# Kernel tuning notes

Measured on AMD Instinct MI355X. Metric: run time of the kernel, lower is better.

The kernel has to match this reference:

```python
import jax, jax.numpy as jnp
import numpy as np
import math

B, H_IM, W_IM, HDIM, HEADS, PS = 16, 56, 56, 512, 8, 7


def setup_inputs() -> dict:
    key = jax.random.key(0)
    ks = jax.random.split(key, 4)
    x = jax.random.normal(ks[0], (B, H_IM * W_IM, HDIM), jnp.float32)
    mask = jnp.zeros((1, 1, H_IM, W_IM), jnp.bool_)
    Wqkv = jax.random.normal(ks[1], (HDIM, 3 * HDIM), jnp.float32) * 0.02
    Wproj = jax.random.normal(ks[2], (HDIM, HDIM), jnp.float32) * 0.02
    bproj = jnp.zeros((HDIM,), jnp.float32)
    rel_bias = jax.random.normal(ks[3], (HEADS, PS * PS, PS * PS), jnp.float32) * 0.02
    return {"x": x, "mask": mask, "Wqkv": Wqkv, "Wproj": Wproj,
            "bproj": bproj, "rel_bias": rel_bias, "H": H_IM, "W": W_IM}


def reference(x, mask, Wqkv, Wproj, bproj, rel_bias, H, W):
    b = x.shape[0]
    ps, g, hd = PS, HEADS, HDIM
    dh = hd // g
    scale = dh ** (-0.5)

    qkv = x @ Wqkv                                   # [b, H*W, 3*hd]
    qkv = qkv.reshape(b, H, W, 3 * hd)
    pad_b = int(math.ceil(H / ps)) * ps - H
    pad_r = int(math.ceil(W / ps)) * ps - W
    qkv = jnp.pad(qkv, ((0, 0), (0, pad_b), (0, pad_r), (0, 0)))
    kmask = jnp.pad(mask, ((0, 0), (0, 0), (0, pad_b), (0, pad_r)), constant_values=True)
    Hp, Wp = H + pad_b, W + pad_r
    sh, sw = Hp // ps, Wp // ps
    K, P = ps * ps, sh * sw

    # patchify: b (sh kh) (sw kw) c -> b (kh kw) (sh sw) c
    qkv = qkv.reshape(b, sh, ps, sw, ps, 3 * hd).transpose(0, 2, 4, 1, 3, 5).reshape(b, K, P, 3 * hd)
    kmask = kmask.reshape(1, 1, sh, ps, sw, ps).transpose(0, 1, 3, 5, 2, 4).reshape(1, 1, K, P)

    qkv = qkv.reshape(b, K, P, 3, g, dh)
    q, k, v = qkv[:, :, :, 0], qkv[:, :, :, 1], qkv[:, :, :, 2]  # each [b, K, P, g, dh]

    attn = jnp.einsum('bqpgc,bkpgc->bgqkp', q, k)    # [b, g, K, K, P]
    attn = (attn + rel_bias[None, :, :, :, None]) * scale
    m = kmask[:, None]                                # [1, 1, 1, K, P]
    attn = jnp.where(m, -jnp.inf, attn)
    attn = jax.nn.softmax(attn, axis=-2)              # softmax over key positions within window
    attn = jnp.where(m, 0.0, attn)

    out = jnp.einsum('bgqkp,bkpgc->bqpgc', attn, v)
    out = out.reshape(b, K, P, hd)
    # un-patchify: b (kh kw) (sh sw) c -> b (sh kh) (sw kw) c
    out = out.reshape(b, ps, ps, sh, sw, hd).transpose(0, 3, 1, 4, 2, 5).reshape(b, Hp, Wp, hd)
    out = out[:, :H, :W, :].reshape(b, H * W, hd)
    return out @ Wproj + bproj
```

## Files before the change

### kernel.cpp

```cpp
#include <hip/hip_runtime.h>
#include <hip/hip_bf16.h>

using bf16 = __hip_bfloat16;
using bf16x8 = __attribute__((ext_vector_type(8))) short;
using f32x4  = __attribute__((ext_vector_type(4))) float;

#define B_    16
#define HIM   56
#define WIM   56
#define HD    512
#define NHEAD 8
#define DH    64
#define NTOK  (HIM*WIM)
#define M_    (B_*NTOK)
#define K49   49

__device__ __forceinline__ void gload_lds16(const void* g, void* l) {
  __builtin_amdgcn_global_load_lds(
      (__attribute__((address_space(1))) const void*)g,
      (__attribute__((address_space(3))) void*)l, 16, 0, 0);
}

__global__ __launch_bounds__(256) void cvt_x_kernel(const float* __restrict__ in,
                                                    bf16* __restrict__ out) {
  size_t i = ((size_t)blockIdx.x * 256 + threadIdx.x) * 8;
  float4 a = *(const float4*)(in + i);
  float4 b = *(const float4*)(in + i + 4);
  union { uint4 v; bf16 h[8]; } o;
  o.h[0] = __float2bfloat16(a.x); o.h[1] = __float2bfloat16(a.y);
  o.h[2] = __float2bfloat16(a.z); o.h[3] = __float2bfloat16(a.w);
  o.h[4] = __float2bfloat16(b.x); o.h[5] = __float2bfloat16(b.y);
  o.h[6] = __float2bfloat16(b.z); o.h[7] = __float2bfloat16(b.w);
  *(uint4*)(out + i) = o.v;
}

__global__ __launch_bounds__(256) void cvt_transpose_kernel(const float* __restrict__ in,
                                                            bf16* __restrict__ out,
                                                            int K, int N) {
  int idx = blockIdx.x * 256 + threadIdx.x;
  int k = idx / N, n = idx - k * N;
  out[(size_t)n * K + k] = __float2bfloat16(in[idx]);
}

template<bool OUT_BF16, bool BIAS>
__global__ __launch_bounds__(256) void gemm128_kernel(
    const bf16* __restrict__ A,
    const bf16* __restrict__ Bt,
    void* __restrict__ Cp,
    const float* __restrict__ bias,
    int M, int N, int K)
{
  __shared__ alignas(16) bf16 lds[2][2][128 * 32];
  const int tid  = threadIdx.x;
  const int lane = tid & 63, wid = tid >> 6;
  const int l15  = lane & 15, kq = lane >> 4;
  const int wm   = wid >> 1,  wn = wid & 1;
  const long arow0 = (long)blockIdx.y * 128;
  const long bcol0 = (long)blockIdx.x * 128;

  auto stage = [&](int buf, int kt) {
    const bf16* gA = A  + arow0 * K + kt * 32;
    const bf16* gB = Bt + bcol0 * K + kt * 32;
#pragma unroll
    for (int c = 0; c < 2; ++c) {
      int s   = c * 256 + tid;
      int row = s >> 2, sl = s & 3;
      int gs  = sl ^ ((row >> 1) & 3);
      const char* pa = (const char*)(gA + (long)row * K) + gs * 16;
      const char* pb = (const char*)(gB + (long)row * K) + gs * 16;
      bf16* la = (bf16*)&lds[buf][0][(c * 256 + wid * 64) * 8];
      bf16* lb = (bf16*)&lds[buf][1][(c * 256 + wid * 64) * 8];
      gload_lds16(pa, la);
      gload_lds16(pb, lb);
    }
  };

  f32x4 acc[4][4] = {};
  stage(0, 0);
  __syncthreads();
  const int nk = K >> 5;
  int buf = 0;
#pragma unroll 1
  for (int kt = 0; kt < nk; ++kt) {
    if (kt + 1 < nk) stage(buf ^ 1, kt + 1);
    bf16x8 af[4], br[4];
#pragma unroll
    for (int mt = 0; mt < 4; ++mt) {
      int row  = wm * 64 + mt * 16 + l15;
      int slot = kq ^ ((row >> 1) & 3);
      af[mt] = *(const bf16x8*)&lds[buf][0][row * 32 + slot * 8];
    }
#pragma unroll
    for (int nt = 0; nt < 4; ++nt) {
      int row  = wn * 64 + nt * 16 + l15;
      int slot = kq ^ ((row >> 1) & 3);
      br[nt] = *(const bf16x8*)&lds[buf][1][row * 32 + slot * 8];
    }
#pragma unroll
    for (int mt = 0; mt < 4; ++mt)
#pragma unroll
      for (int nt = 0; nt < 4; ++nt)
        acc[mt][nt] = __builtin_amdgcn_mfma_f32_16x16x32_bf16(af[mt], br[nt], acc[mt][nt], 0, 0, 0);
    __syncthreads();
    buf ^= 1;
  }

  const long crow0 = arow0 + wm * 64;
  const long ccol0 = bcol0 + wn * 64;
#pragma unroll
  for (int mt = 0; mt < 4; ++mt) {
#pragma unroll
    for (int nt = 0; nt < 4; ++nt) {
      long col = ccol0 + nt * 16 + l15;
      float bv = BIAS ? bias[col] : 0.f;
#pragma unroll
      for (int r = 0; r < 4; ++r) {
        long row = crow0 + mt * 16 + kq * 4 + r;
        if (OUT_BF16)
          ((bf16*)Cp)[row * N + col] = __float2bfloat16(acc[mt][nt][r]);
        else
          ((float*)Cp)[row * N + col] = acc[mt][nt][r] + bv;
      }
    }
  }
}

__global__ __launch_bounds__(256) void attn_win_kernel(
    const bf16* __restrict__ qkv, const float* __restrict__ rb, bf16* __restrict__ outa)
{
  __shared__ alignas(16) bf16 Qs[64 * 72];
  __shared__ alignas(16) bf16 Ks[64 * 72];
  __shared__ alignas(16) bf16 Vt[64 * 72];
  __shared__ alignas(16) bf16 Ps[64 * 72];
  const int tid = threadIdx.x, lane = tid & 63, wid = tid >> 6;
  const int p = blockIdx.x, g = blockIdx.y, b = blockIdx.z;
  const int sh = p >> 3, sw = p & 7;
  const size_t nb = (size_t)b * NTOK;
  const int c8 = (tid & 7) * 8;

#pragma unroll
  for (int it = 0; it < 2; ++it) {
    int t = (tid >> 3) + it * 32;
    uint4 vq = {0, 0, 0, 0}, vk = vq, vv = vq;
    if (t < K49) {
      int ph = t / 7, pw = t - ph * 7;
      int n = (sh * 7 + ph) * WIM + sw * 7 + pw;
      const bf16* src = qkv + (nb + n) * 1536 + g * 64 + c8;
      vq = *(const uint4*)(src);
      vk = *(const uint4*)(src + 512);
      vv = *(const uint4*)(src + 1024);
    }
    *(uint4*)&Qs[t * 72 + c8] = vq;
    *(uint4*)&Ks[t * 72 + c8] = vk;
    union { uint4 u; unsigned short s[8]; } uv; uv.u = vv;
    unsigned short* vt16 = (unsigned short*)Vt;
#pragma unroll
    for (int e = 0; e < 8; ++e) vt16[(c8 + e) * 72 + t] = uv.s[e];
  }
  __syncthreads();

  const int l15 = lane & 15, kq = lane >> 4;
  bf16x8 aq[2];
#pragma unroll
  for (int kk = 0; kk < 2; ++kk)
    aq[kk] = *(const bf16x8*)&Qs[(wid * 16 + l15) * 72 + kk * 32 + kq * 8];
  float sv[4][4];
#pragma unroll
  for (int ct = 0; ct < 4; ++ct) {
    f32x4 acc = {0.f, 0.f, 0.f, 0.f};
#pragma unroll
    for (int kk = 0; kk < 2; ++kk) {
      bf16x8 bk = *(const bf16x8*)&Ks[(ct * 16 + l15) * 72 + kk * 32 + kq * 8];
      acc = __builtin_amdgcn_mfma_f32_16x16x32_bf16(aq[kk], bk, acc, 0, 0, 0);
    }
    int kcol = ct * 16 + l15;
#pragma unroll
    for (int r = 0; r < 4; ++r) {
      int q = wid * 16 + kq * 4 + r;
      float bias = (q < K49 && kcol < K49) ? rb[((size_t)g * K49 + q) * K49 + kcol] : 0.f;
      float v = (acc[r] + bias) * 0.125f;
      sv[ct][r] = (kcol < K49) ? v : -1e30f;
    }
  }
#pragma unroll
  for (int r = 0; r < 4; ++r) {
    float m = fmaxf(fmaxf(sv[0][r], sv[1][r]), fmaxf(sv[2][r], sv[3][r]));
#pragma unroll
    for (int d = 1; d < 16; d <<= 1) m = fmaxf(m, __shfl_xor(m, d));
    float e0 = __expf(sv[0][r] - m), e1 = __expf(sv[1][r] - m);
    float e2 = __expf(sv[2][r] - m), e3 = __expf(sv[3][r] - m);
    float s = e0 + e1 + e2 + e3;
#pragma unroll
    for (int d = 1; d < 16; d <<= 1) s += __shfl_xor(s, d);
    float inv = 1.0f / s;
    int q = wid * 16 + kq * 4 + r;
    Ps[q * 72 +  0 + l15] = __float2bfloat16(e0 * inv);
    Ps[q * 72 + 16 + l15] = __float2bfloat16(e1 * inv);
    Ps[q * 72 + 32 + l15] = __float2bfloat16(e2 * inv);
    Ps[q * 72 + 48 + l15] = __float2bfloat16(e3 * inv);
  }
  __syncthreads();
  bf16x8 ap[2];
#pragma unroll
  for (int kk = 0; kk < 2; ++kk)
    ap[kk] = *(const bf16x8*)&Ps[(wid * 16 + l15) * 72 + kk * 32 + kq * 8];
#pragma unroll
  for (int ct = 0; ct < 4; ++ct) {
    f32x4 acc = {0.f, 0.f, 0.f, 0.f};
#pragma unroll
    for (int kk = 0; kk < 2; ++kk) {
      bf16x8 bv = *(const bf16x8*)&Vt[(ct * 16 + l15) * 72 + kk * 32 + kq * 8];
      acc = __builtin_amdgcn_mfma_f32_16x16x32_bf16(ap[kk], bv, acc, 0, 0, 0);
    }
#pragma unroll
    for (int r = 0; r < 4; ++r) {
      int q = wid * 16 + kq * 4 + r;
      if (q < K49) {
        int ph = q / 7, pw = q - ph * 7;
        int n = (sh * 7 + ph) * WIM + sw * 7 + pw;
        outa[(nb + n) * HD + g * 64 + ct * 16 + l15] = __float2bfloat16(acc[r]);
      }
    }
  }
}

extern "C" void kernel_launch(void* const* d_in, const int* in_sizes, int n_in,
                              void* d_out, int out_size, void* d_ws, size_t ws_size,
                              hipStream_t stream) {
  (void)in_sizes; (void)n_in; (void)out_size;
  const float* x     = (const float*)d_in[0];
  const float* wqkv  = (const float*)d_in[2];
  const float* wproj = (const float*)d_in[3];
  const float* bproj = (const float*)d_in[4];
  const float* rb    = (const float*)d_in[5];

  char* ws = (char*)d_ws;
  bf16* x_bf    = (bf16*)(ws);
  bf16* wqkv_t  = (bf16*)(ws + 51380224);
  bf16* wproj_t = (bf16*)(ws + 52953088);
  bf16* qkv     = (bf16*)(ws + 53477376);
  bf16* attno   = x_bf;
  float* out    = (float*)d_out;
  if (ws_size < 207618048) return;

  cvt_x_kernel<<<dim3(12544), 256, 0, stream>>>(x, x_bf);
  cvt_transpose_kernel<<<dim3(3072), 256, 0, stream>>>(wqkv, wqkv_t, 512, 1536);
  cvt_transpose_kernel<<<dim3(1024), 256, 0, stream>>>(wproj, wproj_t, 512, 512);
  gemm128_kernel<true, false><<<dim3(12, 392), 256, 0, stream>>>(
      x_bf, wqkv_t, (void*)qkv, nullptr, M_, 1536, 512);
  attn_win_kernel<<<dim3(64, NHEAD, B_), 256, 0, stream>>>(qkv, rb, attno);
  gemm128_kernel<false, true><<<dim3(4, 392), 256, 0, stream>>>(
      attno, wproj_t, (void*)out, bproj, M_, 512, 512);
}
```

Baseline: 254.5 us.

## Triple-buffer GEMM pipeline with XCD-aware block remap and nontemporal stores

The GEMM kernel moves from double to triple LDS buffering, prefetching two k-tiles ahead and waiting with explicit vmcnt counts before a single barrier per iteration, in place of two syncthreads. The 2D grid becomes a 1D grid remapped so that consecutive tiles land on the same XCD, to improve L2 reuse. It also raises wave priority around the MFMA block and writes outputs with nontemporal stores. The costs are extra LDS per block (48KB, still within 3 blocks/CU) and reliance on hand-written waitcnt counts being correct.

```diff
diff --git a/kernel.cpp b/kernel.cpp
--- a/kernel.cpp
+++ b/kernel.cpp
@@ -43,20 +43,23 @@
 }
 
 template<bool OUT_BF16, bool BIAS>
-__global__ __launch_bounds__(256) void gemm128_kernel(
+__global__ __launch_bounds__(256, 3) void gemm128_kernel(
     const bf16* __restrict__ A,
     const bf16* __restrict__ Bt,
     void* __restrict__ Cp,
     const float* __restrict__ bias,
-    int M, int N, int K)
+    int M, int N, int K, int NBX)
 {
-  __shared__ alignas(16) bf16 lds[2][2][128 * 32];
+  __shared__ alignas(16) bf16 lds[3][2][128 * 32];
   const int tid  = threadIdx.x;
   const int lane = tid & 63, wid = tid >> 6;
   const int l15  = lane & 15, kq = lane >> 4;
   const int wm   = wid >> 1,  wn = wid & 1;
-  const long arow0 = (long)blockIdx.y * 128;
-  const long bcol0 = (long)blockIdx.x * 128;
+  const int cpx = gridDim.x >> 3;
+  const int wg  = (blockIdx.x & 7) * cpx + (blockIdx.x >> 3);
+  const int by  = wg / NBX, bx = wg - by * NBX;
+  const long arow0 = (long)by * 128;
+  const long bcol0 = (long)bx * 128;
 
   auto stage = [&](int buf, int kt) {
     const bf16* gA = A  + arow0 * K + kt * 32;
@@ -66,43 +69,47 @@
       int s   = c * 256 + tid;
       int row = s >> 2, sl = s & 3;
       int gs  = sl ^ ((row >> 1) & 3);
-      const char* pa = (const char*)(gA + (long)row * K) + gs * 16;
-      const char* pb = (const char*)(gB + (long)row * K) + gs * 16;
-      bf16* la = (bf16*)&lds[buf][0][(c * 256 + wid * 64) * 8];
-      bf16* lb = (bf16*)&lds[buf][1][(c * 256 + wid * 64) * 8];
-      gload_lds16(pa, la);
-      gload_lds16(pb, lb);
+      gload_lds16((const char*)(gA + (long)row * K) + gs * 16,
+                  (bf16*)&lds[buf][0][(c * 256 + wid * 64) * 8]);
+      gload_lds16((const char*)(gB + (long)row * K) + gs * 16,
+                  (bf16*)&lds[buf][1][(c * 256 + wid * 64) * 8]);
     }
   };
 
   f32x4 acc[4][4] = {};
+  const int NT = K >> 5;
   stage(0, 0);
-  __syncthreads();
-  const int nk = K >> 5;
-  int buf = 0;
+  stage(1, 1);
+  int cur = 0;
 #pragma unroll 1
-  for (int kt = 0; kt < nk; ++kt) {
-    if (kt + 1 < nk) stage(buf ^ 1, kt + 1);
+  for (int t = 0; t < NT; ++t) {
+    if (t + 1 < NT) asm volatile("s_waitcnt vmcnt(4)" ::: "memory");
+    else            asm volatile("s_waitcnt vmcnt(0)" ::: "memory");
+    __builtin_amdgcn_s_barrier();
+    asm volatile("" ::: "memory");
+    if (t + 2 < NT) { int nb = cur + 2; if (nb >= 3) nb -= 3; stage(nb, t + 2); }
+
     bf16x8 af[4], br[4];
 #pragma unroll
     for (int mt = 0; mt < 4; ++mt) {
       int row  = wm * 64 + mt * 16 + l15;
       int slot = kq ^ ((row >> 1) & 3);
-      af[mt] = *(const bf16x8*)&lds[buf][0][row * 32 + slot * 8];
-    }
-#pragma unroll
-    for (int nt = 0; nt < 4; ++nt) {
-      int row  = wn * 64 + nt * 16 + l15;
+      af[mt] = *(const bf16x8*)&lds[cur][0][row * 32 + slot * 8];
+    }
+#pragma unroll
+    for (int nt2 = 0; nt2 < 4; ++nt2) {
+      int row  = wn * 64 + nt2 * 16 + l15;
       int slot = kq ^ ((row >> 1) & 3);
-      br[nt] = *(const bf16x8*)&lds[buf][1][row * 32 + slot * 8];
-    }
+      br[nt2] = *(const bf16x8*)&lds[cur][1][row * 32 + slot * 8];
+    }
+    __builtin_amdgcn_s_setprio(1);
 #pragma unroll
     for (int mt = 0; mt < 4; ++mt)
 #pragma unroll
-      for (int nt = 0; nt < 4; ++nt)
-        acc[mt][nt] = __builtin_amdgcn_mfma_f32_16x16x32_bf16(af[mt], br[nt], acc[mt][nt], 0, 0, 0);
-    __syncthreads();
-    buf ^= 1;
+      for (int nt2 = 0; nt2 < 4; ++nt2)
+        acc[mt][nt2] = __builtin_amdgcn_mfma_f32_16x16x32_bf16(af[mt], br[nt2], acc[mt][nt2], 0, 0, 0);
+    __builtin_amdgcn_s_setprio(0);
+    ++cur; if (cur >= 3) cur = 0;
   }
 
   const long crow0 = arow0 + wm * 64;
@@ -110,16 +117,19 @@
 #pragma unroll
   for (int mt = 0; mt < 4; ++mt) {
 #pragma unroll
-    for (int nt = 0; nt < 4; ++nt) {
-      long col = ccol0 + nt * 16 + l15;
+    for (int nt2 = 0; nt2 < 4; ++nt2) {
+      long col = ccol0 + nt2 * 16 + l15;
       float bv = BIAS ? bias[col] : 0.f;
 #pragma unroll
       for (int r = 0; r < 4; ++r) {
         long row = crow0 + mt * 16 + kq * 4 + r;
-        if (OUT_BF16)
-          ((bf16*)Cp)[row * N + col] = __float2bfloat16(acc[mt][nt][r]);
-        else
-          ((float*)Cp)[row * N + col] = acc[mt][nt][r] + bv;
+        if (OUT_BF16) {
+          bf16 h = __float2bfloat16(acc[mt][nt2][r]);
+          __builtin_nontemporal_store(*(const unsigned short*)&h,
+                                      (unsigned short*)Cp + row * N + col);
+        } else {
+          __builtin_nontemporal_store(acc[mt][nt2][r] + bv, (float*)Cp + row * N + col);
+        }
       }
     }
   }
@@ -246,9 +256,9 @@
   cvt_x_kernel<<<dim3(12544), 256, 0, stream>>>(x, x_bf);
   cvt_transpose_kernel<<<dim3(3072), 256, 0, stream>>>(wqkv, wqkv_t, 512, 1536);
   cvt_transpose_kernel<<<dim3(1024), 256, 0, stream>>>(wproj, wproj_t, 512, 512);
-  gemm128_kernel<true, false><<<dim3(12, 392), 256, 0, stream>>>(
-      x_bf, wqkv_t, (void*)qkv, nullptr, M_, 1536, 512);
+  gemm128_kernel<true, false><<<dim3(4704), 256, 0, stream>>>(
+      x_bf, wqkv_t, (void*)qkv, nullptr, M_, 1536, 512, 12);
   attn_win_kernel<<<dim3(64, NHEAD, B_), 256, 0, stream>>>(qkv, rb, attno);
-  gemm128_kernel<false, true><<<dim3(4, 392), 256, 0, stream>>>(
-      attno, wproj_t, (void*)out, bproj, M_, 512, 512);
-}
+  gemm128_kernel<false, true><<<dim3(1568), 256, 0, stream>>>(
+      attno, wproj_t, (void*)out, bproj, M_, 512, 512, 4);
+}
```

Measured after the change: 250.9 us. No clear change (-1.4%).

## Replace 128x128 GEMM with persistent 256x256-tile GEMM and 4-stage pipeline

Applied to the files above, without the earlier changes.

Both linear projections now use a persistent kernel launched with 256 blocks of 1024 threads. Each block walks a contiguous range of 256x256 output tiles, with K fixed at 512. Global-to-LDS loads run through a 4-slot ring that keeps several k-steps in flight, controlled by explicit vmcnt waits and raw barriers, and MFMA sections get raised wave priority. The MFMA operands are swapped so each lane holds four consecutive output columns. That allows vectorised nontemporal stores, and the bias is folded into the accumulator at initialisation. The goal is more data reuse per tile, hidden load latency, and fewer launch and store costs. In exchange it needs 128KB of LDS per block, hand-tuned wait counts that depend on how many stores are outstanding, and uneven tile counts across blocks (1176 tiles over 256 blocks).

```diff
diff --git a/kernel.cpp b/kernel.cpp
--- a/kernel.cpp
+++ b/kernel.cpp
@@ -42,84 +42,111 @@
   out[(size_t)n * K + k] = __float2bfloat16(in[idx]);
 }
 
-template<bool OUT_BF16, bool BIAS>
-__global__ __launch_bounds__(256) void gemm128_kernel(
+template<int N, bool OUT_BF16, bool BIAS>
+__global__ __launch_bounds__(1024, 4) void gemm_persist_kernel(
     const bf16* __restrict__ A,
     const bf16* __restrict__ Bt,
     void* __restrict__ Cp,
     const float* __restrict__ bias,
-    int M, int N, int K)
+    int NBX, int NTILES)
 {
-  __shared__ alignas(16) bf16 lds[2][2][128 * 32];
+  constexpr int K = 512;
+  __shared__ alignas(16) bf16 lds[2][4][256 * 32];
   const int tid  = threadIdx.x;
   const int lane = tid & 63, wid = tid >> 6;
   const int l15  = lane & 15, kq = lane >> 4;
-  const int wm   = wid >> 1,  wn = wid & 1;
-  const long arow0 = (long)blockIdx.y * 128;
-  const long bcol0 = (long)blockIdx.x * 128;
-
-  auto stage = [&](int buf, int kt) {
-    const bf16* gA = A  + arow0 * K + kt * 32;
-    const bf16* gB = Bt + bcol0 * K + kt * 32;
-#pragma unroll
-    for (int c = 0; c < 2; ++c) {
-      int s   = c * 256 + tid;
-      int row = s >> 2, sl = s & 3;
-      int gs  = sl ^ ((row >> 1) & 3);
-      const char* pa = (const char*)(gA + (long)row * K) + gs * 16;
-      const char* pb = (const char*)(gB + (long)row * K) + gs * 16;
-      bf16* la = (bf16*)&lds[buf][0][(c * 256 + wid * 64) * 8];
-      bf16* lb = (bf16*)&lds[buf][1][(c * 256 + wid * 64) * 8];
-      gload_lds16(pa, la);
-      gload_lds16(pb, lb);
-    }
+  const int wm   = wid >> 2,  wn = wid & 3;
+
+  const int bid  = blockIdx.x, nb = gridDim.x;
+  int cnt = NTILES / nb;
+  const int rem = NTILES - cnt * nb;
+  const int tstart = bid * cnt + (bid < rem ? bid : rem);
+  if (bid < rem) ++cnt;
+  const int smax = cnt * 16;
+
+  f32x4 vb[2][4];
+  if (BIAS) {
+#pragma unroll
+    for (int x = 0; x < 2; ++x)
+#pragma unroll
+      for (int nt = 0; nt < 4; ++nt)
+        vb[x][nt] = *(const f32x4*)&bias[x * 256 + wn * 64 + nt * 16 + kq * 4];
+  }
+
+  auto stageS = [&](int s) {
+    const int tt = tstart + (s >> 4);
+    const int j  = s & 15;
+    const int by = tt / NBX, bx = tt - by * NBX;
+    const bf16* gA = A  + (long)by * 256 * K + j * 32;
+    const bf16* gB = Bt + (long)bx * 256 * K + j * 32;
+    const int row = tid >> 2, sl = tid & 3;
+    const int gs  = sl ^ ((row >> 1) & 3);
+    gload_lds16((const char*)(gA + (long)row * K) + gs * 16, &lds[0][s & 3][wid * 64 * 8]);
+    gload_lds16((const char*)(gB + (long)row * K) + gs * 16, &lds[1][s & 3][wid * 64 * 8]);
   };
 
-  f32x4 acc[4][4] = {};
-  stage(0, 0);
-  __syncthreads();
-  const int nk = K >> 5;
-  int buf = 0;
+  stageS(0); stageS(1); stageS(2);
+
+  int s = 0;
 #pragma unroll 1
-  for (int kt = 0; kt < nk; ++kt) {
-    if (kt + 1 < nk) stage(buf ^ 1, kt + 1);
-    bf16x8 af[4], br[4];
+  for (int tl = 0; tl < cnt; ++tl) {
+    f32x4 acc[4][4];
+    const int tt = tstart + tl;
+    const int bxt = tt - (tt / NBX) * NBX;
+#pragma unroll
+    for (int mt = 0; mt < 4; ++mt)
+#pragma unroll
+      for (int nt = 0; nt < 4; ++nt)
+        acc[mt][nt] = BIAS ? vb[bxt][nt] : f32x4{0.f, 0.f, 0.f, 0.f};
+
+#pragma unroll 1
+    for (int j = 0; j < 16; ++j, ++s) {
+      if (tl > 0 && j < 3)   asm volatile("s_waitcnt vmcnt(20)" ::: "memory");
+      else if (s == smax - 2) asm volatile("s_waitcnt vmcnt(2)"  ::: "memory");
+      else if (s == smax - 1) asm volatile("s_waitcnt vmcnt(0)"  ::: "memory");
+      else                    asm volatile("s_waitcnt vmcnt(4)"  ::: "memory");
+      __builtin_amdgcn_s_barrier();
+      if (s + 3 < smax) stageS(s + 3);
+      const int sl4 = s & 3;
+      bf16x8 bb[4];
+#pragma unroll
+      for (int nt = 0; nt < 4; ++nt) {
+        int row = wn * 64 + nt * 16 + l15;
+        bb[nt] = *(const bf16x8*)&lds[1][sl4][row * 32 + ((kq ^ ((row >> 1) & 3)) << 3)];
+      }
+      __builtin_amdgcn_s_setprio(1);
+#pragma unroll
+      for (int mt = 0; mt < 4; ++mt) {
+        int row = wm * 64 + mt * 16 + l15;
+        bf16x8 af = *(const bf16x8*)&lds[0][sl4][row * 32 + ((kq ^ ((row >> 1) & 3)) << 3)];
+#pragma unroll
+        for (int nt = 0; nt < 4; ++nt)
+          acc[mt][nt] = __builtin_amdgcn_mfma_f32_16x16x32_bf16(bb[nt], af, acc[mt][nt], 0, 0, 0);
+      }
+      __builtin_amdgcn_s_setprio(0);
+    }
+
+    const int byt = tt / NBX;
+    const long crow0 = (long)byt * 256 + wm * 64;
+    const long ccol0 = (long)bxt * 256 + wn * 64 + kq * 4;
 #pragma unroll
     for (int mt = 0; mt < 4; ++mt) {
-      int row  = wm * 64 + mt * 16 + l15;
-      int slot = kq ^ ((row >> 1) & 3);
-      af[mt] = *(const bf16x8*)&lds[buf][0][row * 32 + slot * 8];
-    }
-#pragma unroll
-    for (int nt = 0; nt < 4; ++nt) {
-      int row  = wn * 64 + nt * 16 + l15;
-      int slot = kq ^ ((row >> 1) & 3);
-      br[nt] = *(const bf16x8*)&lds[buf][1][row * 32 + slot * 8];
-    }
-#pragma unroll
-    for (int mt = 0; mt < 4; ++mt)
-#pragma unroll
-      for (int nt = 0; nt < 4; ++nt)
-        acc[mt][nt] = __builtin_amdgcn_mfma_f32_16x16x32_bf16(af[mt], br[nt], acc[mt][nt], 0, 0, 0);
-    __syncthreads();
-    buf ^= 1;
-  }
-
-  const long crow0 = arow0 + wm * 64;
-  const long ccol0 = bcol0 + wn * 64;
-#pragma unroll
-  for (int mt = 0; mt < 4; ++mt) {
-#pragma unroll
-    for (int nt = 0; nt < 4; ++nt) {
-      long col = ccol0 + nt * 16 + l15;
-      float bv = BIAS ? bias[col] : 0.f;
-#pragma unroll
-      for (int r = 0; r < 4; ++r) {
-        long row = crow0 + mt * 16 + kq * 4 + r;
-        if (OUT_BF16)
-          ((bf16*)Cp)[row * N + col] = __float2bfloat16(acc[mt][nt][r]);
-        else
-          ((float*)Cp)[row * N + col] = acc[mt][nt][r] + bv;
+      long row = crow0 + mt * 16 + l15;
+#pragma unroll
+      for (int nt = 0; nt < 4; ++nt) {
+        long col = ccol0 + nt * 16;
+        if (OUT_BF16) {
+          union { unsigned long long u; unsigned short h[4]; } pk;
+#pragma unroll
+          for (int r = 0; r < 4; ++r) {
+            bf16 hh = __float2bfloat16(acc[mt][nt][r]);
+            pk.h[r] = *(unsigned short*)&hh;
+          }
+          __builtin_nontemporal_store(pk.u,
+              (unsigned long long*)((bf16*)Cp + row * N + col));
+        } else {
+          __builtin_nontemporal_store(acc[mt][nt], (f32x4*)((float*)Cp + row * N + col));
+        }
       }
     }
   }
@@ -246,9 +273,9 @@
   cvt_x_kernel<<<dim3(12544), 256, 0, stream>>>(x, x_bf);
   cvt_transpose_kernel<<<dim3(3072), 256, 0, stream>>>(wqkv, wqkv_t, 512, 1536);
   cvt_transpose_kernel<<<dim3(1024), 256, 0, stream>>>(wproj, wproj_t, 512, 512);
-  gemm128_kernel<true, false><<<dim3(12, 392), 256, 0, stream>>>(
-      x_bf, wqkv_t, (void*)qkv, nullptr, M_, 1536, 512);
+  gemm_persist_kernel<1536, true, false><<<dim3(256), 1024, 0, stream>>>(
+      x_bf, wqkv_t, (void*)qkv, nullptr, 6, 1176);
   attn_win_kernel<<<dim3(64, NHEAD, B_), 256, 0, stream>>>(qkv, rb, attno);
-  gemm128_kernel<false, true><<<dim3(4, 392), 256, 0, stream>>>(
-      attno, wproj_t, (void*)out, bproj, M_, 512, 512);
-}
+  gemm_persist_kernel<512, false, true><<<dim3(256), 1024, 0, stream>>>(
+      attno, wproj_t, (void*)out, bproj, 2, 392);
+}
```

Measured after the change: 265.9 us. 4.5% more time.
